# Optimization experiments

Measured on AMD Instinct MI355X. Metric: run time of the kernel, lower is better.

## Reference

```python
import jax, jax.numpy as jnp
import numpy as np

N_NODES = 20000
N_EDGES = 200000
D_IN, D_H1, D_H2, D_OUT = 1433, 1000, 500, 7


def setup_inputs() -> dict:
    key = jax.random.key(0)
    ks = jax.random.split(key, 8)
    features = jax.random.normal(ks[0], (N_NODES, D_IN), dtype=jnp.float32)
    src = jax.random.randint(ks[1], (N_EDGES,), 0, N_NODES)
    dst = jax.random.randint(ks[2], (N_EDGES,), 0, N_NODES)
    W1 = jax.random.normal(ks[3], (D_IN, D_H1), dtype=jnp.float32) * 0.02
    b1 = jnp.zeros((D_H1,), dtype=jnp.float32)
    W2 = jax.random.normal(ks[4], (D_H1, D_H2), dtype=jnp.float32) * 0.02
    b2 = jnp.zeros((D_H2,), dtype=jnp.float32)
    W3 = jax.random.normal(ks[5], (D_H2, D_OUT), dtype=jnp.float32) * 0.02
    b3 = jnp.zeros((D_OUT,), dtype=jnp.float32)
    return {"features": features, "src": src, "dst": dst,
            "W1": W1, "b1": b1, "W2": W2, "b2": b2, "W3": W3, "b3": b3}


def reference(features, src, dst, W1, b1, W2, b2, W3, b3):
    N = features.shape[0]

    def agg(x):  # sum_tensors over incoming neighbors: h_i = sum_{(j->i) in E} x_j
        return jax.ops.segment_sum(x[src], dst, num_segments=N)

    # GCN layer 1: aggregate -> linear -> relu
    x = jax.nn.relu(agg(features) @ W1 + b1)       # [N, 1000]
    # GCN layer 2: aggregate -> linear -> relu (dropout = identity in eval)
    x = jax.nn.relu(agg(x) @ W2 + b2)              # [N, 500]
    # output linear -> relu (dropout = identity in eval)
    x = jax.nn.relu(x @ W3 + b3)                   # [N, 7]
    return x
```

## Files before the change

kernel.cpp:

```cpp
#include <hip/hip_runtime.h>
#include <hip/hip_bf16.h>


#define N_NODES 20000
#define N_EDGES 200000
#define D_IN    1433
#define D_H1    1000
#define D_H2    500
#define D_OUT   7

#define MPAD    20096
#define K1PAD   1472
#define N1PAD   1024
#define K2PAD   1024
#define N2PAD   512
#define MBLK    157
#define SCAN_N  (N_NODES + 1)
#define TB1     ((N1PAD / 32) * (K1PAD / 32))
#define TB2     ((N2PAD / 32) * (K2PAD / 32))
#define CNTB    ((N_EDGES + 255) / 256)
#define NCHUNK1 16
#define NB4     (MPAD / 4)

typedef __attribute__((ext_vector_type(8))) short short8;
typedef __attribute__((ext_vector_type(8))) unsigned short ushort8_t;
typedef __attribute__((ext_vector_type(4))) float f32x4;

__device__ __forceinline__ unsigned short bf16_rne(float x) {
    unsigned int u = __float_as_uint(x);
    u = (u + 0x7FFFu + ((u >> 16) & 1u)) >> 16;
    return (unsigned short)u;
}
__device__ __forceinline__ float bf16_up(unsigned short h) {
    return __uint_as_float((unsigned int)h << 16);
}

__device__ __forceinline__ void gl_lds16(const unsigned short* g, unsigned short* lds) {
    __builtin_amdgcn_global_load_lds(
        (const __attribute__((address_space(1))) unsigned int*)g,
        (__attribute__((address_space(3))) unsigned int*)lds, 16, 0, 0);
}

__global__ __launch_bounds__(256) void prep(const float* __restrict__ F,
                                            unsigned int* __restrict__ Fout,
                                            const float* __restrict__ W1,
                                            unsigned short* __restrict__ W1T,
                                            const float* __restrict__ W2,
                                            unsigned short* __restrict__ W2T,
                                            const int* __restrict__ dst,
                                            int* __restrict__ offs) {
    __shared__ float tile[32][33];
    const int bid = blockIdx.x, t = threadIdx.x;
    if (bid < MPAD) {
        int e = bid * 256 + t;
        if (e < N_EDGES) atomicAdd(&offs[dst[e] + 1], 1);
        const float* fr = F + (size_t)bid * D_IN;
        bool live = bid < N_NODES;
        for (int kk = t; kk < K1PAD / 2; kk += 256) {
            int k0 = kk * 2;
            float a = (live && k0     < D_IN) ? fr[k0]     : 0.f;
            float b = (live && k0 + 1 < D_IN) ? fr[k0 + 1] : 0.f;
            Fout[(size_t)bid * (K1PAD / 2) + kk] =
                (unsigned int)bf16_rne(a) | ((unsigned int)bf16_rne(b) << 16);
        }
        return;
    }
    const float* src; unsigned short* dstp;
    int SR, SC, DR, DC, bx, by;
    if (bid < MPAD + TB1) {
        int l = bid - MPAD;
        bx = l % (N1PAD / 32); by = l / (N1PAD / 32);
        src = W1; dstp = W1T; SR = D_IN; SC = D_H1; DR = N1PAD; DC = K1PAD;
    } else {
        int l = bid - MPAD - TB1;
        bx = l % (N2PAD / 32); by = l / (N2PAD / 32);
        src = W2; dstp = W2T; SR = D_H1; SC = D_H2; DR = N2PAD; DC = K2PAD;
    }
    const int c0 = bx * 32, r0 = by * 32;
    const int tx = t & 31, ty = t >> 5;
    #pragma unroll
    for (int p = 0; p < 4; ++p) {
        int r = r0 + ty + p * 8, c = c0 + tx;
        tile[ty + p * 8][tx] = (r < SR && c < SC) ? src[(size_t)r * SC + c] : 0.f;
    }
    __syncthreads();
    #pragma unroll
    for (int p = 0; p < 4; ++p) {
        int dr = c0 + ty + p * 8;
        int dc = r0 + tx;
        if (dr < DR && dc < DC) dstp[(size_t)dr * DC + dc] = bf16_rne(tile[tx][ty + p * 8]);
    }
}

__global__ __launch_bounds__(1024) void scan_csr(int* __restrict__ offs) {
    __shared__ int wsum[16];
    const int t = threadIdx.x, lane = t & 63, wv = t >> 6;
    const int base = t * 20;
    int v[20];
    int run = 0;
    #pragma unroll
    for (int k = 0; k < 20; ++k) {
        int i = base + k;
        int x = (i < SCAN_N) ? offs[i] : 0;
        run += x;
        v[k] = run;
    }
    const int tot = run;
    int w = tot;
    #pragma unroll
    for (int s = 1; s < 64; s <<= 1) {
        int u = __shfl_up(w, s, 64);
        if (lane >= s) w += u;
    }
    if (lane == 63) wsum[wv] = w;
    __syncthreads();
    int prefix = w - tot;
    for (int k = 0; k < wv; ++k) prefix += wsum[k];
    #pragma unroll
    for (int k = 0; k < 20; ++k) {
        int i = base + k;
        if (i < SCAN_N) offs[i] = prefix + v[k];
    }
}

__global__ __launch_bounds__(256) void fill_csr(const int* __restrict__ src,
                                                const int* __restrict__ dst,
                                                int* __restrict__ offs,
                                                int* __restrict__ srcs) {
    int e = blockIdx.x * 256 + threadIdx.x;
    if (e < N_EDGES) {
        int pos = atomicAdd(&offs[dst[e]], 1);
        srcs[pos] = src[e];
    }
}

template <int KPAD, int NB>
__global__ __launch_bounds__(256) void gemm_mfma(const unsigned short* __restrict__ A,
                                                 const unsigned short* __restrict__ B,
                                                 unsigned short* __restrict__ C,
                                                 int M, int OSTR) {
    __shared__ __align__(16) unsigned short sA[128 * 64];
    __shared__ __align__(16) unsigned short sB[128 * 64];
    const int bid = blockIdx.x;
    const int xcd = bid & 7;
    const int tt  = bid >> 3;
    const int nb  = tt % NB;
    const int mb  = (tt / NB) * 8 + xcd;
    if (mb >= MBLK) return;

    const int t = threadIdx.x;
    const int w = t >> 6, lane = t & 63;
    const int m0 = mb * 128, n0 = nb * 128;
    const int wm = (w >> 1) * 64, wn = (w & 1) * 64;

    const int srowo = lane >> 3;
    const int skc   = ((lane & 7) ^ srowo) * 8;
    const int mrow = lane & 15, quad = lane >> 4;

    const unsigned short* Aptr = A + (size_t)(m0 + srowo) * KPAD + skc;
    const unsigned short* Bptr = B + (size_t)(n0 + srowo) * KPAD + skc;

    f32x4 acc[4][4] = {};

    for (int k0 = 0; k0 < KPAD; k0 += 64) {
        #pragma unroll
        for (int c = 0; c < 4; ++c) {
            const int rbase = c * 32 + w * 8;
            gl_lds16(Aptr + (size_t)rbase * KPAD, &sA[rbase * 64]);
            gl_lds16(Bptr + (size_t)rbase * KPAD, &sB[rbase * 64]);
        }
        Aptr += 64; Bptr += 64;
        __syncthreads();

        #pragma unroll
        for (int s = 0; s < 2; ++s) {
            short8 af[4], bf[4];
            #pragma unroll
            for (int mt = 0; mt < 4; ++mt) {
                int r = wm + mt * 16 + mrow;
                af[mt] = *(const short8*)&sA[r * 64 + (((s * 4 + quad) ^ (mrow & 7)) * 8)];
            }
            #pragma unroll
            for (int nt = 0; nt < 4; ++nt) {
                int r = wn + nt * 16 + mrow;
                bf[nt] = *(const short8*)&sB[r * 64 + (((s * 4 + quad) ^ (mrow & 7)) * 8)];
            }
            #pragma unroll
            for (int mt = 0; mt < 4; ++mt)
                #pragma unroll
                for (int nt = 0; nt < 4; ++nt)
                    acc[mt][nt] = __builtin_amdgcn_mfma_f32_16x16x32_bf16(
                        af[mt], bf[nt], acc[mt][nt], 0, 0, 0);
        }
        __syncthreads();
    }

    #pragma unroll
    for (int mt = 0; mt < 4; ++mt) {
        int m = m0 + wm + mt * 16 + quad * 4;
        #pragma unroll
        for (int nt = 0; nt < 4; ++nt) {
            int n = n0 + wn + nt * 16 + mrow;
            if (n >= OSTR) continue;
            #pragma unroll
            for (int r = 0; r < 4; ++r)
                if (m + r < M) C[(size_t)(m + r) * OSTR + n] = bf16_rne(acc[mt][nt][r]);
        }
    }
}

__global__ __launch_bounds__(256) void agg1_chunk(const unsigned short* __restrict__ H,
                                                  const int* __restrict__ offs,
                                                  const int* __restrict__ srcs,
                                                  const float* __restrict__ bias,
                                                  unsigned short* __restrict__ X,
                                                  int hstr) {
    const int bx = blockIdx.x;
    const int c  = bx / NB4;
    const int i  = (bx % NB4) * 4 + (threadIdx.x >> 6);
    const int lane = threadIdx.x & 63;
    const int g = lane >> 3, sub = lane & 7;
    const int c0 = c * 64;
    ushort8_t o = (ushort8_t)0;
    if (i < N_NODES) {
        const int end = offs[i];
        const int beg = i ? offs[i - 1] : 0;
        const unsigned short* Hc = H + c0 + sub * 8;
        float s[8] = {};
        for (int e0 = beg; e0 < end; e0 += 8) {
            int edge = e0 + g;
            if (edge < end) {
                int j = srcs[edge];
                ushort8_t v = *(const ushort8_t*)(Hc + (size_t)j * hstr);
                #pragma unroll
                for (int u = 0; u < 8; ++u) s[u] += bf16_up(v[u]);
            }
        }
        #pragma unroll
        for (int u = 0; u < 8; ++u) {
            s[u] += __shfl_xor(s[u], 8, 64);
            s[u] += __shfl_xor(s[u], 16, 64);
            s[u] += __shfl_xor(s[u], 32, 64);
        }
        if (g == 0) {
            #pragma unroll
            for (int u = 0; u < 8; ++u) {
                int col = c0 + sub * 8 + u;
                float b = (col < D_H1) ? bias[col] : 0.f;
                o[u] = bf16_rne(fmaxf(s[u] + b, 0.f));
            }
        }
    }
    if (g == 0)
        *(ushort8_t*)(X + (size_t)i * K2PAD + c0 + sub * 8) = o;
}

__global__ __launch_bounds__(64) void agg2_out(const unsigned short* __restrict__ H,
                                               const int* __restrict__ offs,
                                               const int* __restrict__ srcs,
                                               const float* __restrict__ b2,
                                               const float* __restrict__ W3,
                                               const float* __restrict__ b3,
                                               float* __restrict__ out,
                                               int hstr) {
    const int i = blockIdx.x, t = threadIdx.x;
    const int tc = t < 63 ? t : 62;
    const int end = offs[i];
    const int beg = i ? offs[i - 1] : 0;
    const unsigned short* Hc = H + tc * 8;
    float s[8] = {};
    int e = beg;
    for (; e + 8 <= end; e += 8) {
        int j0 = srcs[e],     j1 = srcs[e + 1], j2 = srcs[e + 2], j3 = srcs[e + 3];
        int j4 = srcs[e + 4], j5 = srcs[e + 5], j6 = srcs[e + 6], j7 = srcs[e + 7];
        ushort8_t v0 = *(const ushort8_t*)(Hc + (size_t)j0 * hstr);
        ushort8_t v1 = *(const ushort8_t*)(Hc + (size_t)j1 * hstr);
        ushort8_t v2 = *(const ushort8_t*)(Hc + (size_t)j2 * hstr);
        ushort8_t v3 = *(const ushort8_t*)(Hc + (size_t)j3 * hstr);
        ushort8_t v4 = *(const ushort8_t*)(Hc + (size_t)j4 * hstr);
        ushort8_t v5 = *(const ushort8_t*)(Hc + (size_t)j5 * hstr);
        ushort8_t v6 = *(const ushort8_t*)(Hc + (size_t)j6 * hstr);
        ushort8_t v7 = *(const ushort8_t*)(Hc + (size_t)j7 * hstr);
        #pragma unroll
        for (int u = 0; u < 8; ++u) {
            float t0 = (bf16_up(v0[u]) + bf16_up(v1[u])) +
                       (bf16_up(v2[u]) + bf16_up(v3[u]));
            float t1 = (bf16_up(v4[u]) + bf16_up(v5[u])) +
                       (bf16_up(v6[u]) + bf16_up(v7[u]));
            s[u] += t0 + t1;
        }
    }
    for (; e + 4 <= end; e += 4) {
        int j0 = srcs[e], j1 = srcs[e + 1], j2 = srcs[e + 2], j3 = srcs[e + 3];
        ushort8_t v0 = *(const ushort8_t*)(Hc + (size_t)j0 * hstr);
        ushort8_t v1 = *(const ushort8_t*)(Hc + (size_t)j1 * hstr);
        ushort8_t v2 = *(const ushort8_t*)(Hc + (size_t)j2 * hstr);
        ushort8_t v3 = *(const ushort8_t*)(Hc + (size_t)j3 * hstr);
        #pragma unroll
        for (int u = 0; u < 8; ++u)
            s[u] += (bf16_up(v0[u]) + bf16_up(v1[u])) +
                    (bf16_up(v2[u]) + bf16_up(v3[u]));
    }
    for (; e < end; ++e) {
        ushort8_t v = *(const ushort8_t*)(Hc + (size_t)srcs[e] * hstr);
        #pragma unroll
        for (int u = 0; u < 8; ++u) s[u] += bf16_up(v[u]);
    }

    float acc[D_OUT] = {};
    if (t < 63) {
        #pragma unroll
        for (int u = 0; u < 8; ++u) {
            int col = t * 8 + u;
            if (col < D_H2) {
                float x = fmaxf(s[u] + b2[col], 0.f);
                const float* wr = W3 + (size_t)col * D_OUT;
                #pragma unroll
                for (int j = 0; j < D_OUT; ++j) acc[j] += x * wr[j];
            }
        }
    }
    #pragma unroll
    for (int j = 0; j < D_OUT; ++j)
        #pragma unroll
        for (int off = 32; off; off >>= 1) acc[j] += __shfl_down(acc[j], off);
    if (t == 0) {
        #pragma unroll
        for (int j = 0; j < D_OUT; ++j)
            out[(size_t)i * D_OUT + j] = fmaxf(acc[j] + b3[j], 0.f);
    }
}

extern "C" void kernel_launch(void* const* d_in, const int* in_sizes, int n_in,
                              void* d_out, int out_size, void* d_ws, size_t ws_size,
                              hipStream_t stream) {
    const float* features = (const float*)d_in[0];
    const int*   src      = (const int*)d_in[1];
    const int*   dst      = (const int*)d_in[2];
    const float* W1       = (const float*)d_in[3];
    const float* b1       = (const float*)d_in[4];
    const float* W2       = (const float*)d_in[5];
    const float* b2       = (const float*)d_in[6];
    const float* W3       = (const float*)d_in[7];
    const float* b3       = (const float*)d_in[8];
    float* out = (float*)d_out;

    const size_t FBF_B  = (size_t)MPAD * K1PAD * 2;
    const size_t W1T_B  = (size_t)N1PAD * K1PAD * 2;
    const size_t W2T_B  = (size_t)N2PAD * K2PAD * 2;
    const size_t OFFS_B = (size_t)SCAN_N * 4;
    const size_t bigNeed = FBF_B + (size_t)N_NODES * 1088 * 2 + W1T_B + W2T_B + OFFS_B;
    const bool big = ws_size >= bigNeed;
    const int h1str = big ? 1088 : 1008;
    const int h2str = big ? 576  : 504;

    char* ws = (char*)d_ws;
    unsigned short* Fbf  = (unsigned short*)(ws + 0);
    unsigned short* X1bf = (unsigned short*)(ws + 0);
    unsigned short* H1   = (unsigned short*)(ws + FBF_B);
    unsigned short* H2   = (unsigned short*)(ws + FBF_B);
    size_t oW1T = FBF_B + (size_t)N_NODES * h1str * 2;
    unsigned short* W1T  = (unsigned short*)(ws + oW1T);
    unsigned short* W2T  = (unsigned short*)(ws + oW1T + W1T_B);
    int* offs = (int*)(ws + oW1T + W1T_B + W2T_B);
    int* srcs = (int*)(ws + oW1T);

    hipMemsetAsync(offs, 0, SCAN_N * sizeof(int), stream);

    prep<<<MPAD + TB1 + TB2, 256, 0, stream>>>(
        features, (unsigned int*)Fbf, W1, W1T, W2, W2T, dst, offs);

    scan_csr<<<1, 1024, 0, stream>>>(offs);

    gemm_mfma<K1PAD, N1PAD / 128><<<8 * (N1PAD / 128) * 20, 256, 0, stream>>>(
        Fbf, W1T, H1, N_NODES, h1str);

    fill_csr<<<CNTB, 256, 0, stream>>>(src, dst, offs, srcs);

    agg1_chunk<<<NCHUNK1 * NB4, 256, 0, stream>>>(H1, offs, srcs, b1, X1bf, h1str);

    gemm_mfma<K2PAD, N2PAD / 128><<<8 * (N2PAD / 128) * 20, 256, 0, stream>>>(
        X1bf, W2T, H2, N_NODES, h2str);

    agg2_out<<<N_NODES, 64, 0, stream>>>(H2, offs, srcs, b2, W3, b3, out, h2str);
}
```

Measured before the change: 489.2 us.

## Aggregate layer-1 rows with one wavefront per node and batched gathers

Replaces the chunked layer-1 aggregation, which launched 16 column-chunk blocks per group of four nodes with 8-lane edge groups and shuffle reductions, with one 64-thread block per node. Each lane covers 16 columns across all edges, and the edge loop is unrolled by 8 and 4 so several gathered row loads are in flight at once. This drops the cross-lane reductions and the repeated reads of CSR offsets and sources per chunk. In exchange each node's edges are processed serially by a single wave, which adds latency for high-degree nodes and lowers the number of independent blocks.

```diff
diff --git a/kernel.cpp b/kernel.cpp
--- a/kernel.cpp
+++ b/kernel.cpp
@@ -19,8 +19,6 @@
 #define TB1     ((N1PAD / 32) * (K1PAD / 32))
 #define TB2     ((N2PAD / 32) * (K2PAD / 32))
 #define CNTB    ((N_EDGES + 255) / 256)
-#define NCHUNK1 16
-#define NB4     (MPAD / 4)
 
 typedef __attribute__((ext_vector_type(8))) short short8;
 typedef __attribute__((ext_vector_type(8))) unsigned short ushort8_t;
@@ -209,50 +207,82 @@
     }
 }
 
-__global__ __launch_bounds__(256) void agg1_chunk(const unsigned short* __restrict__ H,
-                                                  const int* __restrict__ offs,
-                                                  const int* __restrict__ srcs,
-                                                  const float* __restrict__ bias,
-                                                  unsigned short* __restrict__ X,
-                                                  int hstr) {
-    const int bx = blockIdx.x;
-    const int c  = bx / NB4;
-    const int i  = (bx % NB4) * 4 + (threadIdx.x >> 6);
-    const int lane = threadIdx.x & 63;
-    const int g = lane >> 3, sub = lane & 7;
-    const int c0 = c * 64;
-    ushort8_t o = (ushort8_t)0;
+__global__ __launch_bounds__(64) void agg1_bf16(const unsigned short* __restrict__ H,
+                                                const int* __restrict__ offs,
+                                                const int* __restrict__ srcs,
+                                                const float* __restrict__ bias,
+                                                unsigned short* __restrict__ X,
+                                                int hstr) {
+    const int i = blockIdx.x, tc = threadIdx.x;
+    ushort8_t olo = (ushort8_t)0, ohi = (ushort8_t)0;
     if (i < N_NODES) {
         const int end = offs[i];
         const int beg = i ? offs[i - 1] : 0;
-        const unsigned short* Hc = H + c0 + sub * 8;
-        float s[8] = {};
-        for (int e0 = beg; e0 < end; e0 += 8) {
-            int edge = e0 + g;
-            if (edge < end) {
-                int j = srcs[edge];
-                ushort8_t v = *(const ushort8_t*)(Hc + (size_t)j * hstr);
+        const unsigned short* Hc = H + tc * 16;
+        float s[16] = {};
+        int e = beg;
+        for (; e + 8 <= end; e += 8) {
+            int j[8];
+            #pragma unroll
+            for (int q = 0; q < 8; ++q) j[q] = srcs[e + q];
+            ushort8_t vl[8], vh[8];
+            #pragma unroll
+            for (int q = 0; q < 8; ++q) {
+                const unsigned short* p = Hc + (size_t)j[q] * hstr;
+                vl[q] = *(const ushort8_t*)p;
+                vh[q] = *(const ushort8_t*)(p + 8);
+            }
+            #pragma unroll
+            for (int q = 0; q < 8; ++q) {
                 #pragma unroll
-                for (int u = 0; u < 8; ++u) s[u] += bf16_up(v[u]);
+                for (int u = 0; u < 8; ++u) {
+                    s[u]     += bf16_up(vl[q][u]);
+                    s[u + 8] += bf16_up(vh[q][u]);
+                }
+            }
+        }
+        for (; e + 4 <= end; e += 4) {
+            int j[4];
+            #pragma unroll
+            for (int q = 0; q < 4; ++q) j[q] = srcs[e + q];
+            ushort8_t vl[4], vh[4];
+            #pragma unroll
+            for (int q = 0; q < 4; ++q) {
+                const unsigned short* p = Hc + (size_t)j[q] * hstr;
+                vl[q] = *(const ushort8_t*)p;
+                vh[q] = *(const ushort8_t*)(p + 8);
+            }
+            #pragma unroll
+            for (int q = 0; q < 4; ++q) {
+                #pragma unroll
+                for (int u = 0; u < 8; ++u) {
+                    s[u]     += bf16_up(vl[q][u]);
+                    s[u + 8] += bf16_up(vh[q][u]);
+                }
+            }
+        }
+        for (; e < end; ++e) {
+            const unsigned short* p = Hc + (size_t)srcs[e] * hstr;
+            ushort8_t vl = *(const ushort8_t*)p;
+            ushort8_t vh = *(const ushort8_t*)(p + 8);
+            #pragma unroll
+            for (int u = 0; u < 8; ++u) {
+                s[u]     += bf16_up(vl[u]);
+                s[u + 8] += bf16_up(vh[u]);
             }
         }
         #pragma unroll
         for (int u = 0; u < 8; ++u) {
-            s[u] += __shfl_xor(s[u], 8, 64);
-            s[u] += __shfl_xor(s[u], 16, 64);
-            s[u] += __shfl_xor(s[u], 32, 64);
-        }
-        if (g == 0) {
-            #pragma unroll
-            for (int u = 0; u < 8; ++u) {
-                int col = c0 + sub * 8 + u;
-                float b = (col < D_H1) ? bias[col] : 0.f;
-                o[u] = bf16_rne(fmaxf(s[u] + b, 0.f));
-            }
-        }
-    }
-    if (g == 0)
-        *(ushort8_t*)(X + (size_t)i * K2PAD + c0 + sub * 8) = o;
+            int cl = tc * 16 + u, ch = cl + 8;
+            float bl = (cl < D_H1) ? bias[cl] : 0.f;
+            float bh = (ch < D_H1) ? bias[ch] : 0.f;
+            olo[u] = (cl < D_H1) ? bf16_rne(fmaxf(s[u] + bl, 0.f)) : (unsigned short)0;
+            ohi[u] = (ch < D_H1) ? bf16_rne(fmaxf(s[u + 8] + bh, 0.f)) : (unsigned short)0;
+        }
+    }
+    unsigned short* xp = X + (size_t)i * K2PAD + tc * 16;
+    *(ushort8_t*)xp = olo;
+    *(ushort8_t*)(xp + 8) = ohi;
 }
 
 __global__ __launch_bounds__(64) void agg2_out(const unsigned short* __restrict__ H,
@@ -377,7 +407,7 @@
 
     fill_csr<<<CNTB, 256, 0, stream>>>(src, dst, offs, srcs);
 
-    agg1_chunk<<<NCHUNK1 * NB4, 256, 0, stream>>>(H1, offs, srcs, b1, X1bf, h1str);
+    agg1_bf16<<<MPAD, 64, 0, stream>>>(H1, offs, srcs, b1, X1bf, h1str);
 
     gemm_mfma<K2PAD, N2PAD / 128><<<8 * (N2PAD / 128) * 20, 256, 0, stream>>>(
         X1bf, W2T, H2, N_NODES, h2str);
```

Measured after the change: 430.3 us. 12.0% less time.
